# Optimization experiments

Measured on AMD Instinct MI355X. Metric: run time of the kernel, lower is better.

## Reference

```python
import jax, jax.numpy as jnp
import numpy as np

D_MODEL = 1024
NUM_HEADS = 16
D_K = D_MODEL // NUM_HEADS
ROPE_THETA = 10000.0


def _rope(x, positions):
    # x: [B, H, S, Dk]; positions: [S] int. Interleaved-pair RoPE, theta=10000.
    half = D_K // 2
    inv_freq = 1.0 / (ROPE_THETA ** (jnp.arange(half, dtype=jnp.float32) * 2.0 / D_K))
    ang = positions.astype(jnp.float32)[:, None] * inv_freq[None, :]  # [S, half]
    cos = jnp.cos(ang)[None, None]  # [1,1,S,half]
    sin = jnp.sin(ang)[None, None]
    x_even = x[..., 0::2]
    x_odd = x[..., 1::2]
    r_even = x_even * cos - x_odd * sin
    r_odd = x_even * sin + x_odd * cos
    out = jnp.stack([r_even, r_odd], axis=-1)  # [B,H,S,half,2]
    return out.reshape(x.shape)


def setup_inputs() -> dict:
    key = jax.random.key(0)
    ks = jax.random.split(key, 5)
    B, S = 4, 2048
    std = (2.0 / (D_MODEL + D_MODEL)) ** 0.5
    return {
        "x": jax.random.normal(ks[0], (B, S, D_MODEL), dtype=jnp.float32),
        "Wq": jax.random.normal(ks[1], (D_MODEL, D_MODEL), dtype=jnp.float32) * std,
        "Wk": jax.random.normal(ks[2], (D_MODEL, D_MODEL), dtype=jnp.float32) * std,
        "Wv": jax.random.normal(ks[3], (D_MODEL, D_MODEL), dtype=jnp.float32) * std,
        "Wo": jax.random.normal(ks[4], (D_MODEL, D_MODEL), dtype=jnp.float32) * std,
        "token_positions": jnp.arange(S, dtype=jnp.int32),
    }


def reference(x, Wq, Wk, Wv, Wo, token_positions):
    B, S, _ = x.shape
    # QKV projections (weights stored [out, in], y = x @ W^T)
    def proj(W):
        y = jnp.einsum('bsi,oi->bso', x, W)
        return y.reshape(B, S, NUM_HEADS, D_K).transpose(0, 2, 1, 3)  # [B,H,S,Dk]
    q = _rope(proj(Wq), token_positions)
    k = _rope(proj(Wk), token_positions)
    v = proj(Wv)
    scores = jnp.einsum('bhqd,bhkd->bhqk', q, k) / jnp.sqrt(jnp.float32(D_K))
    causal = token_positions[:, None] >= token_positions[None, :]  # [S,S]
    scores = jnp.where(causal[None, None], scores, jnp.float32(-1e9))
    probs = jax.nn.softmax(scores, axis=-1)
    attn = jnp.einsum('bhqk,bhkd->bhqd', probs, v)
    attn = attn.transpose(0, 2, 1, 3).reshape(B, S, D_MODEL)
    return jnp.einsum('bsi,oi->bso', attn, Wo)
```

## Files before the change

### kernel.cpp

```cpp
#include <hip/hip_runtime.h>
#include <hip/hip_bf16.h>
#include <math.h>

#define SEQ 2048
#define BATCH 4
#define MROWS (BATCH*SEQ)
#define DMODEL 1024
#define NHEADS 16
#define DKH 64

typedef float f32x4 __attribute__((ext_vector_type(4)));
typedef float f32x16 __attribute__((ext_vector_type(16)));
typedef __bf16 bf16x8 __attribute__((ext_vector_type(8)));
typedef unsigned short u16;
typedef unsigned int u32;
typedef u16 u16x4 __attribute__((ext_vector_type(4)));
typedef u16 u16x8 __attribute__((ext_vector_type(8)));
typedef u32 u32x4v __attribute__((ext_vector_type(4)));

__device__ __forceinline__ u16 f2bf(float f) {
  union { float f; unsigned u; } v; v.f = f;
  unsigned r = v.u + 0x7FFFu + ((v.u >> 16) & 1u);
  return (u16)(r >> 16);
}

__device__ __forceinline__ void async_copy16(const void* g, void* l) {
  __builtin_amdgcn_global_load_lds(
      (const __attribute__((address_space(1))) void*)g,
      (__attribute__((address_space(3))) void*)l, 16, 0, 0);
}

__device__ __forceinline__ u32 cvtpk(float lo, float hi) {
  u32 r;
  asm("v_cvt_pk_bf16_f32 %0, %1, %2" : "=v"(r) : "v"(lo), "v"(hi));
  return r;
}

__global__ __launch_bounds__(256) void k_prep(
    const float* __restrict__ x,
    const float* __restrict__ Wq, const float* __restrict__ Wk,
    const float* __restrict__ Wv, const float* __restrict__ Wo,
    const int* __restrict__ pos,
    u16* __restrict__ xb, u16* __restrict__ Wqb, u16* __restrict__ Wkb,
    u16* __restrict__ Wvb, u16* __restrict__ Wob,
    float2* __restrict__ csT)
{
  const int bid = blockIdx.x, tid = threadIdx.x;
  if (bid < 8192) {
    int i = bid*256 + tid;
    float4 v = ((const float4*)x)[i];
    u16x4 o; o[0]=f2bf(v.x); o[1]=f2bf(v.y); o[2]=f2bf(v.z); o[3]=f2bf(v.w);
    ((u16x4*)xb)[i] = o;
  } else if (bid < 12288) {
    int wi = (bid - 8192) >> 10;
    const float* src = (wi==0)?Wq:(wi==1)?Wk:(wi==2)?Wv:Wo;
    u16* dst = (wi==0)?Wqb:(wi==1)?Wkb:(wi==2)?Wvb:Wob;
    int i = ((bid - 8192) & 1023)*256 + tid;
    float4 v = ((const float4*)src)[i];
    u16x4 o; o[0]=f2bf(v.x); o[1]=f2bf(v.y); o[2]=f2bf(v.z); o[3]=f2bf(v.w);
    ((u16x4*)dst)[i] = o;
  } else {
    int i = (bid - 12288)*256 + tid;
    int s = i >> 5, j = i & 31;
    float p = (float)pos[s];
    float inv = __builtin_exp2f((float)j * -0.4152410118f);
    float a = p * inv;
    csT[i] = make_float2(__cosf(a), __sinf(a));
  }
}

template<int MODE>
__global__ __launch_bounds__(512, 4) void k_g5(
    const u16* __restrict__ A,
    const u16* __restrict__ W0, const u16* __restrict__ W1,
    const u16* __restrict__ W2,
    u16* __restrict__ Qo, u16* __restrict__ Ko, u16* __restrict__ Vto,
    float* __restrict__ Fo,
    const float2* __restrict__ csT)
{
  __shared__ alignas(16) u16 Asl[128*64];
  __shared__ alignas(16) u16 Bsl[128*64];

  const int bm = blockIdx.x, y = blockIdx.y;
  int proj, bnl;
  const u16* W;
  if constexpr (MODE == 0) {
    proj = y >> 3; bnl = y & 7;
    W = (proj == 0) ? W0 : (proj == 1) ? W1 : W2;
  } else {
    proj = 3; bnl = y; W = W0;
  }

  const int tid = threadIdx.x;
  const int wave = tid >> 6, lane = tid & 63;
  const int lg = lane >> 4, lr = lane & 15;
  const int wm = wave >> 2, wn = wave & 3;

  const u16* Ab = A + (size_t)(bm*128)*DMODEL;
  const u16* Wb = W + (size_t)(bnl*128)*DMODEL;

  f32x4 acc[4][2];
#pragma unroll
  for (int i = 0; i < 4; ++i)
#pragma unroll
    for (int j = 0; j < 2; ++j) acc[i][j] = (f32x4){0,0,0,0};

  for (int t = 0; t < 16; ++t) {
    const int k0 = t * 64;
#pragma unroll
    for (int i = 0; i < 2; ++i) {
      const int idx = i*512 + tid;
      const int row = idx >> 3, ch = idx & 7;
      const int sc = (ch ^ (row & 7)) * 8;
      async_copy16(Ab + (size_t)row*DMODEL + k0 + sc, (char*)Asl + idx*16);
      async_copy16(Wb + (size_t)row*DMODEL + k0 + sc, (char*)Bsl + idx*16);
    }
    __syncthreads();
#pragma unroll
    for (int kk = 0; kk < 2; ++kk) {
      bf16x8 bfr[2];
#pragma unroll
      for (int ni = 0; ni < 2; ++ni) {
        const int row = wn*32 + ni*16 + lr;
        bfr[ni] = *(const bf16x8*)&Bsl[row*64 + (((kk*4 + lg) ^ (row & 7)) * 8)];
      }
#pragma unroll
      for (int mi = 0; mi < 4; ++mi) {
        const int row = wm*64 + mi*16 + lr;
        bf16x8 af = *(const bf16x8*)&Asl[row*64 + (((kk*4 + lg) ^ (row & 7)) * 8)];
#pragma unroll
        for (int ni = 0; ni < 2; ++ni)
          acc[mi][ni] = __builtin_amdgcn_mfma_f32_16x16x32_bf16(af, bfr[ni], acc[mi][ni], 0, 0, 0);
      }
    }
    __syncthreads();
  }

#pragma unroll
  for (int mi = 0; mi < 4; ++mi) {
    const int row0 = bm*128 + wm*64 + mi*16 + lg*4;
#pragma unroll
    for (int ni = 0; ni < 2; ++ni) {
      const int col = bnl*128 + wn*32 + ni*16 + lr;
      f32x4 a = acc[mi][ni];
      if constexpr (MODE == 1) {
#pragma unroll
        for (int r = 0; r < 4; ++r) Fo[(size_t)(row0+r)*DMODEL + col] = a[r];
      } else {
        if (proj == 2) {
          const int hh = col >> 6, dd = col & 63;
          const int s0r = row0 & (SEQ-1);
          const int bb = row0 >> 11;
          u16x4 wv;
#pragma unroll
          for (int r = 0; r < 4; ++r) wv[r] = f2bf(a[r]);
          *(u16x4*)&Vto[((size_t)((bb*16+hh)*64 + dd))*SEQ + s0r] = wv;
        } else {
          u16* C = (proj == 0) ? Qo : Ko;
          const float scl = (proj == 0) ? 0.18033688f : 1.0f;
          const int dd = col & 63;
          const int jj = dd >> 1;
          const float sgn = (dd & 1) ? 1.0f : -1.0f;
#pragma unroll
          for (int r = 0; r < 4; ++r) {
            const int s = (row0 + r) & (SEQ-1);
            float v = a[r];
            float pv = __shfl_xor(v, 1, 64);
            float2 cs = csT[s*32 + jj];
            C[(size_t)(row0+r)*DMODEL + col] = f2bf((v*cs.x + sgn*pv*cs.y) * scl);
          }
        }
      }
    }
  }
}

__global__ __launch_bounds__(512) void k_attn(
    const u16* __restrict__ Q, const u16* __restrict__ K,
    const u16* __restrict__ Vt, u16* __restrict__ O)
{
  const int B = blockIdx.x;
  const int bh = ((B & 7) << 3) | ((B >> 3) & 7);
  const int qt = 7 - (B >> 6);
  const int b = bh >> 4, h = bh & 15;
  const int wave = threadIdx.x >> 6, lane = threadIdx.x & 63;
  const int ql = lane & 31, hi = lane >> 5, hi4 = hi * 4;
  const int R0 = qt*256 + wave*32;

  __shared__ alignas(16) u16 Ks[2][64*64];
  __shared__ alignas(16) u16 Vs[2][64*64];

  const u16* Qb = Q + (size_t)(b*SEQ)*DMODEL + h*64;
  const u16* Kb = K + (size_t)(b*SEQ)*DMODEL + h*64;
  const u16* Vb = Vt + (size_t)(bh*64)*SEQ;

  bf16x8 qf[4];
#pragma unroll
  for (int j = 0; j < 4; ++j)
    qf[j] = *(const bf16x8*)(Qb + (size_t)(R0 + ql)*DMODEL + j*16 + hi*8);

  union { u16x8 u; bf16x8 v; } onesu;
#pragma unroll
  for (int i = 0; i < 8; ++i) onesu.u[i] = 0x3F80;
  const bf16x8 ones = onesu.v;

  f32x16 o0 = (f32x16)(0.f), o1 = (f32x16)(0.f);
  f32x16 lacc = (f32x16)(0.f);

  const int KT = (qt + 1) * 4;
  const int qp = (ql & ~12) | ((ql & 4) << 1) | ((ql & 8) >> 1);

  auto stage = [&](int buf, int kt) {
    const int idx = threadIdx.x;
    const int row = idx >> 3, ch = idx & 7;
    const int sch = (ch ^ (row & 7)) * 8;
    const int k0 = kt * 64;
    async_copy16(Kb + (size_t)(k0 + row)*DMODEL + sch, (char*)Ks[buf] + idx*16);
    async_copy16(Vb + (size_t)row*SEQ + k0 + sch,      (char*)Vs[buf] + idx*16);
  };

  stage(0, 0);
  __syncthreads();

  for (int kt = 0; kt < KT; ++kt) {
    const int cur = kt & 1;
    if (kt + 1 < KT) stage(cur ^ 1, kt + 1);

    const int k0 = kt*64;
    if (k0 <= R0 + 31) {
      const u16* Kw = Ks[cur];
      const u16* Vw = Vs[cur];

      bf16x8 ka[2][4];
#pragma unroll
      for (int st = 0; st < 2; ++st)
#pragma unroll
        for (int j = 0; j < 4; ++j) {
          const int rk = st*32 + qp;
          const int c = (2*j + hi) ^ (rk & 7);
          ka[st][j] = *(const bf16x8*)&Kw[rk*64 + c*8];
        }
      f32x16 s0 = (f32x16)(0.f), s1 = (f32x16)(0.f);
#pragma unroll
      for (int j = 0; j < 4; ++j) {
        s0 = __builtin_amdgcn_mfma_f32_32x32x16_bf16(ka[0][j], qf[j], s0, 0, 0, 0);
        s1 = __builtin_amdgcn_mfma_f32_32x32x16_bf16(ka[1][j], qf[j], s1, 0, 0, 0);
      }

      if (k0 + 63 > R0) {
        const int base = k0 - R0;
#pragma unroll
        for (int r = 0; r < 16; ++r) {
          const int kl = (r & 7) + (hi << 3) + ((r & 8) << 1);
          s0[r] = (ql >= base + kl)      ? s0[r] : -1e30f;
          s1[r] = (ql >= base + 32 + kl) ? s1[r] : -1e30f;
        }
      }

      bf16x8 pb[4];
#pragma unroll
      for (int sl = 0; sl < 4; ++sl) {
        const f32x16& s = (sl < 2) ? s0 : s1;
        const int o8 = (sl & 1) * 8;
        u32 w0 = cvtpk(__builtin_exp2f(s[o8+0]), __builtin_exp2f(s[o8+1]));
        u32 w1 = cvtpk(__builtin_exp2f(s[o8+2]), __builtin_exp2f(s[o8+3]));
        u32 w2 = cvtpk(__builtin_exp2f(s[o8+4]), __builtin_exp2f(s[o8+5]));
        u32 w3 = cvtpk(__builtin_exp2f(s[o8+6]), __builtin_exp2f(s[o8+7]));
        union { u32x4v u; bf16x8 v; } uu;
        uu.u = (u32x4v){w0, w1, w2, w3};
        pb[sl] = uu.v;
      }

#pragma unroll
      for (int sl = 0; sl < 4; ++sl) {
        const int c0 = 2*sl + hi;
        const int d0 = ql,      ca = (c0 ^ (d0 & 7));
        const int d1 = 32 + ql, cb = (c0 ^ (d1 & 7));
        bf16x8 va0 = *(const bf16x8*)&Vw[d0*64 + ca*8];
        bf16x8 va1 = *(const bf16x8*)&Vw[d1*64 + cb*8];
        o0 = __builtin_amdgcn_mfma_f32_32x32x16_bf16(va0, pb[sl], o0, 0, 0, 0);
        o1 = __builtin_amdgcn_mfma_f32_32x32x16_bf16(va1, pb[sl], o1, 0, 0, 0);
        lacc = __builtin_amdgcn_mfma_f32_32x32x16_bf16(ones, pb[sl], lacc, 0, 0, 0);
      }
    }
    __syncthreads();
  }

  const float inv = 1.0f / lacc[0];
  u16* Orow = O + (size_t)(b*SEQ + R0 + ql)*DMODEL + h*64;
#pragma unroll
  for (int rb = 0; rb < 4; ++rb) {
    u16x4 wA, wB;
#pragma unroll
    for (int j = 0; j < 4; ++j) {
      wA[j] = f2bf(o0[rb*4 + j] * inv);
      wB[j] = f2bf(o1[rb*4 + j] * inv);
    }
    *(u16x4*)(Orow + 8*rb + hi4)      = wA;
    *(u16x4*)(Orow + 32 + 8*rb + hi4) = wB;
  }
}

extern "C" void kernel_launch(void* const* d_in, const int* in_sizes, int n_in,
                              void* d_out, int out_size, void* d_ws, size_t ws_size,
                              hipStream_t stream) {
  const float* x  = (const float*)d_in[0];
  const float* Wq = (const float*)d_in[1];
  const float* Wk = (const float*)d_in[2];
  const float* Wv = (const float*)d_in[3];
  const float* Wo = (const float*)d_in[4];
  const int* pos  = (const int*)d_in[5];
  float* out = (float*)d_out;

  const size_t SZ_X   = (size_t)MROWS*DMODEL*2;
  const size_t SZ_W   = (size_t)DMODEL*DMODEL*2;
  const size_t SZ_TAB = (size_t)SEQ*32*8;
  char* w = (char*)d_ws;
  u16* xb   = (u16*)(w);
  u16* Wqb  = (u16*)(w + SZ_X);
  u16* Wkb  = (u16*)(w + SZ_X + SZ_W);
  u16* Wvb  = (u16*)(w + SZ_X + 2*SZ_W);
  u16* Wob  = (u16*)(w + SZ_X + 3*SZ_W);
  float2* csT = (float2*)(w + SZ_X + 4*SZ_W);
  u16* Qb   = (u16*)(w + SZ_X + 4*SZ_W + SZ_TAB);
  u16* Kb   = (u16*)(w + 2*SZ_X + 4*SZ_W + SZ_TAB);
  u16* Ob   = (u16*)(w + 3*SZ_X + 4*SZ_W + SZ_TAB);
  u16* Vt   = (u16*)(w + 4*SZ_X + 4*SZ_W + SZ_TAB);
  const size_t need = 5*SZ_X + 4*SZ_W + SZ_TAB;
  if (ws_size < need) return;

  k_prep<<<12544, 256, 0, stream>>>(x, Wq, Wk, Wv, Wo, pos,
                                    xb, Wqb, Wkb, Wvb, Wob, csT);
  k_g5<0><<<dim3(64, 24), 512, 0, stream>>>(
      xb, Wqb, Wkb, Wvb, Qb, Kb, Vt, nullptr, csT);
  k_attn<<<512, 512, 0, stream>>>(Qb, Kb, Vt, Ob);
  k_g5<1><<<dim3(64, 8), 512, 0, stream>>>(
      Ob, Wob, nullptr, nullptr, nullptr, nullptr, nullptr, out, csT);
}
```

Before: 174.9 us.

## Split attention key range across two blocks and add a combine kernel

```diff
diff --git a/kernel.cpp b/kernel.cpp
--- a/kernel.cpp
+++ b/kernel.cpp
@@ -22,6 +22,10 @@
   union { float f; unsigned u; } v; v.f = f;
   unsigned r = v.u + 0x7FFFu + ((v.u >> 16) & 1u);
   return (u16)(r >> 16);
+}
+__device__ __forceinline__ float bf2f(u16 b) {
+  union { unsigned u; float f; } v; v.u = ((unsigned)b) << 16;
+  return v.f;
 }
 
 __device__ __forceinline__ void async_copy16(const void* g, void* l) {
@@ -177,11 +181,14 @@
 
 __global__ __launch_bounds__(512) void k_attn(
     const u16* __restrict__ Q, const u16* __restrict__ K,
-    const u16* __restrict__ Vt, u16* __restrict__ O)
+    const u16* __restrict__ Vt,
+    u16* __restrict__ OA, u16* __restrict__ OB, float* __restrict__ Lp)
 {
   const int B = blockIdx.x;
   const int bh = ((B & 7) << 3) | ((B >> 3) & 7);
-  const int qt = 7 - (B >> 6);
+  const int g = B >> 6;
+  const int qt = 7 - (g >> 1);
+  const int half = g & 1;
   const int b = bh >> 4, h = bh & 15;
   const int wave = threadIdx.x >> 6, lane = threadIdx.x & 63;
   const int ql = lane & 31, hi = lane >> 5, hi4 = hi * 4;
@@ -207,11 +214,12 @@
   f32x16 o0 = (f32x16)(0.f), o1 = (f32x16)(0.f);
   f32x16 lacc = (f32x16)(0.f);
 
-  const int KT = (qt + 1) * 4;
+  const int kt0 = half * 2 * (qt + 1);
+  const int kt1 = kt0 + 2 * (qt + 1);
   const int qp = (ql & ~12) | ((ql & 4) << 1) | ((ql & 8) >> 1);
 
   auto stage = [&](int buf, int kt) {
-    const int idx = threadIdx.x;
+    const int idx = (int)threadIdx.x;
     const int row = idx >> 3, ch = idx & 7;
     const int sch = (ch ^ (row & 7)) * 8;
     const int k0 = kt * 64;
@@ -219,12 +227,12 @@
     async_copy16(Vb + (size_t)row*SEQ + k0 + sch,      (char*)Vs[buf] + idx*16);
   };
 
-  stage(0, 0);
+  stage(0, kt0);
   __syncthreads();
 
-  for (int kt = 0; kt < KT; ++kt) {
-    const int cur = kt & 1;
-    if (kt + 1 < KT) stage(cur ^ 1, kt + 1);
+  for (int kt = kt0; kt < kt1; ++kt) {
+    const int cur = (kt - kt0) & 1;
+    if (kt + 1 < kt1) stage(cur ^ 1, kt + 1);
 
     const int k0 = kt*64;
     if (k0 <= R0 + 31) {
@@ -286,19 +294,43 @@
     __syncthreads();
   }
 
-  const float inv = 1.0f / lacc[0];
-  u16* Orow = O + (size_t)(b*SEQ + R0 + ql)*DMODEL + h*64;
+  u16* Op = half ? OB : OA;
+  u16* Orow = Op + (size_t)(b*SEQ + R0 + ql)*DMODEL + h*64;
 #pragma unroll
   for (int rb = 0; rb < 4; ++rb) {
     u16x4 wA, wB;
 #pragma unroll
     for (int j = 0; j < 4; ++j) {
-      wA[j] = f2bf(o0[rb*4 + j] * inv);
-      wB[j] = f2bf(o1[rb*4 + j] * inv);
+      wA[j] = f2bf(o0[rb*4 + j]);
+      wB[j] = f2bf(o1[rb*4 + j]);
     }
     *(u16x4*)(Orow + 8*rb + hi4)      = wA;
     *(u16x4*)(Orow + 32 + 8*rb + hi4) = wB;
   }
+  if (hi == 0)
+    Lp[half*(64*SEQ) + bh*SEQ + R0 + ql] = lacc[0];
+}
+
+__global__ __launch_bounds__(256) void k_comb(
+    const u16* __restrict__ OA, const u16* __restrict__ OB,
+    const float* __restrict__ Lp, u16* __restrict__ O)
+{
+  const int gid = blockIdx.x*256 + threadIdx.x;
+  const int row = gid >> 7;
+  const int c8  = (gid & 127) * 8;
+  const int h = c8 >> 6;
+  const int bh = (row >> 11)*16 + h;
+  const int qrow = row & (SEQ-1);
+  const float lA = Lp[bh*SEQ + qrow];
+  const float lB = Lp[64*SEQ + bh*SEQ + qrow];
+  const float inv = 1.0f / (lA + lB);
+  u16x8 a = *(const u16x8*)&OA[(size_t)row*DMODEL + c8];
+  u16x8 bb = *(const u16x8*)&OB[(size_t)row*DMODEL + c8];
+  u16x8 o;
+#pragma unroll
+  for (int j = 0; j < 8; ++j)
+    o[j] = f2bf((bf2f(a[j]) + bf2f(bb[j])) * inv);
+  *(u16x8*)&O[(size_t)row*DMODEL + c8] = o;
 }
 
 extern "C" void kernel_launch(void* const* d_in, const int* in_sizes, int n_in,
@@ -333,7 +365,9 @@
                                     xb, Wqb, Wkb, Wvb, Wob, csT);
   k_g5<0><<<dim3(64, 24), 512, 0, stream>>>(
       xb, Wqb, Wkb, Wvb, Qb, Kb, Vt, nullptr, csT);
-  k_attn<<<512, 512, 0, stream>>>(Qb, Kb, Vt, Ob);
+  k_attn<<<1024, 512, 0, stream>>>(Qb, Kb, Vt,
+                                    xb,  Ob,  (float*)Wqb);
+  k_comb<<<4096, 256, 0, stream>>>(xb, Ob, (const float*)Wqb,  Qb);
   k_g5<1><<<dim3(64, 8), 512, 0, stream>>>(
-      Ob, Wob, nullptr, nullptr, nullptr, nullptr, nullptr, out, csT);
-}
+      Qb, Wob, nullptr, nullptr, nullptr, nullptr, nullptr, out, csT);
+}
```

Measured after the change: 187.5 us. 7.2% more time.
